# Optimization experiments

Hardware: AMD Instinct MI355X
Metric: run time of the kernel (lower is better)

## Reference

```python
import jax, jax.numpy as jnp
import numpy as np

B, N, C = 2, 2048, 1024
H = 16
D = C // H  # head_dim = 64

def setup_inputs() -> dict:
    key = jax.random.key(0)
    ks = jax.random.split(key, 5)
    scale = 1.0 / np.sqrt(C)
    return {
        "x": jax.random.normal(ks[0], (B, N, C), dtype=jnp.float32),
        "w_qkv": jax.random.normal(ks[1], (C, 3 * C), dtype=jnp.float32) * scale,
        "b_qkv": jnp.zeros((3 * C,), dtype=jnp.float32),
        "w_out": jax.random.normal(ks[2], (C, C), dtype=jnp.float32) * scale,
        "b_out": jnp.zeros((C,), dtype=jnp.float32),
    }

def reference(x, w_qkv, b_qkv, w_out, b_out):
    b, n, c = x.shape
    # fused QKV projection: [B,N,3C] -> [3,B,H,N,D]
    qkv = (x @ w_qkv + b_qkv).reshape(b, n, 3, H, D).transpose(2, 0, 3, 1, 4)
    q, k, v = qkv[0], qkv[1], qkv[2]
    # scaled dot-product attention (dropout is identity in eval / p=0)
    attn = jnp.einsum('bhqd,bhkd->bhqk', q, k) * (D ** -0.5)
    attn = jax.nn.softmax(attn, axis=-1)
    out = jnp.einsum('bhqk,bhkd->bhqd', attn, v)
    out = out.transpose(0, 2, 1, 3).reshape(b, n, c)
    return out @ w_out + b_out
```

## Files before the change

kernel.cpp:

```cpp
#include <hip/hip_runtime.h>

typedef unsigned short u16;
typedef __bf16 bf16x8 __attribute__((ext_vector_type(8)));
typedef __bf16 bf16x4 __attribute__((ext_vector_type(4)));
typedef float f32x4 __attribute__((ext_vector_type(4)));

#define LOG2E 1.44269504088896340736f

constexpr int Bc = 2, Nc = 2048, Cch = 1024, Hh = 16, Dd = 64;
constexpr int Mrows = Bc * Nc;
constexpr int N_QKV = 3 * Cch;

__device__ __forceinline__ u16 f2bf(float f) {
  unsigned int u = __float_as_uint(f);
  u += 0x7fffu + ((u >> 16) & 1u);
  return (u16)(u >> 16);
}

__device__ __forceinline__ void gload16(const void* g, void* l) {
  __builtin_amdgcn_global_load_lds((const __attribute__((address_space(1))) void*)g,
                                   (__attribute__((address_space(3))) void*)l, 16, 0, 0);
}

#define MFMA(a, b, c) __builtin_amdgcn_mfma_f32_16x16x32_bf16(a, b, c, 0, 0, 0)

__global__ __launch_bounds__(256) void cast_x_kernel(const float* __restrict__ in,
                                                     u16* __restrict__ out, int n4) {
  int i = blockIdx.x * 256 + threadIdx.x;
  if (i >= n4) return;
  float4 v = *(const float4*)&in[i * 4];
  union { u16 h[4]; short4 s; } u;
  u.h[0] = f2bf(v.x); u.h[1] = f2bf(v.y); u.h[2] = f2bf(v.z); u.h[3] = f2bf(v.w);
  *(short4*)&out[i * 4] = u.s;
}

__global__ __launch_bounds__(256) void transpose_cast_kernel(const float* __restrict__ in,
                                                             u16* __restrict__ out,
                                                             int R, int Cq) {
  __shared__ float tile[32][33];
  int bx = blockIdx.x * 32;
  int by = blockIdx.y * 32;
  int tx = threadIdx.x & 31, ty = threadIdx.x >> 5;
#pragma unroll
  for (int i = 0; i < 32; i += 8)
    tile[ty + i][tx] = in[(size_t)(by + ty + i) * Cq + bx + tx];
  __syncthreads();
#pragma unroll
  for (int i = 0; i < 32; i += 8)
    out[(size_t)(bx + ty + i) * R + by + tx] = f2bf(tile[tx][ty + i]);
}

__global__ __launch_bounds__(256) void transpose_v_kernel(const u16* __restrict__ in,
                                                          u16* __restrict__ out) {
  __shared__ u16 tile[32][33];
  int n0 = blockIdx.x * 32, d0 = blockIdx.y * 32;
  size_t base = (size_t)blockIdx.z * 2048 * 64;
  int tx = threadIdx.x & 31, ty = threadIdx.x >> 5;
#pragma unroll
  for (int i = 0; i < 32; i += 8)
    tile[ty + i][tx] = in[base + (size_t)(n0 + ty + i) * 64 + d0 + tx];
  __syncthreads();
#pragma unroll
  for (int i = 0; i < 32; i += 8)
    out[base + (size_t)(d0 + ty + i) * 2048 + n0 + tx] = tile[tx][ty + i];
}

template <int NWG, int NY>
__global__ __launch_bounds__(256) void gemm_qkv_kernel(const u16* __restrict__ A,
                                                       const u16* __restrict__ Bt,
                                                       const float* __restrict__ bias,
                                                       u16* __restrict__ Qo,
                                                       u16* __restrict__ Ko,
                                                       u16* __restrict__ Vo) {
  __shared__ u16 As[128 * 32];
  __shared__ u16 Bs[128 * 32];
  f32x4 acc[4][4] = {};
  int tid = threadIdx.x, lane = tid & 63, wid = tid >> 6;
  int wr = wid >> 1, wc = wid & 1;
  int l15 = lane & 15, g = lane >> 4;
  int wgid = (blockIdx.x & 7) * (NWG >> 3) + (blockIdx.x >> 3);
  int rowBase = (wgid / NY) * 128, colBase = (wgid % NY) * 128;
  int rowS = tid >> 2, c8 = (tid & 3) << 3;

  for (int k0 = 0; k0 < 1024; k0 += 32) {
    __syncthreads();
    gload16(&A[(size_t)(rowBase + rowS) * 1024 + k0 + c8],        (char*)As + wid * 1024);
    gload16(&A[(size_t)(rowBase + 64 + rowS) * 1024 + k0 + c8],   (char*)As + 4096 + wid * 1024);
    gload16(&Bt[(size_t)(colBase + rowS) * 1024 + k0 + c8],       (char*)Bs + wid * 1024);
    gload16(&Bt[(size_t)(colBase + 64 + rowS) * 1024 + k0 + c8],  (char*)Bs + 4096 + wid * 1024);
    __syncthreads();
    bf16x8 af[4], bfv[4];
#pragma unroll
    for (int m = 0; m < 4; ++m)
      af[m] = *(const bf16x8*)&As[(wr * 64 + m * 16 + l15) * 32 + g * 8];
#pragma unroll
    for (int n = 0; n < 4; ++n)
      bfv[n] = *(const bf16x8*)&Bs[(wc * 64 + n * 16 + l15) * 32 + g * 8];
#pragma unroll
    for (int m = 0; m < 4; ++m)
#pragma unroll
      for (int n = 0; n < 4; ++n)
        acc[m][n] = MFMA(af[m], bfv[n], acc[m][n]);
  }

#pragma unroll
  for (int m = 0; m < 4; ++m)
#pragma unroll
    for (int n = 0; n < 4; ++n) {
      int colc = colBase + wc * 64 + n * 16 + l15;
      float bv = bias[colc];
      int s = colc >> 10, hd = colc & 1023;
      int h = hd >> 6, d = hd & 63;
      float scale = (s == 0) ? (0.125f * LOG2E) : 1.0f;
#pragma unroll
      for (int j = 0; j < 4; ++j) {
        int r = rowBase + wr * 64 + m * 16 + g * 4 + j;
        int b = r >> 11, nn = r & 2047;
        u16 v = f2bf((acc[m][n][j] + bv) * scale);
        size_t idx = (((size_t)(b * 16 + h)) * 2048 + nn) * 64 + d;
        if (s == 0)      Qo[idx] = v;
        else if (s == 1) Ko[idx] = v;
        else             Vo[idx] = v;
      }
    }
}

__global__ __launch_bounds__(256) void attn_kernel(const u16* __restrict__ Q,
                                                   const u16* __restrict__ Km,
                                                   const u16* __restrict__ Vt,
                                                   u16* __restrict__ AO) {
  __shared__ u16 KV[16384];
  __shared__ u16 Ps[128 * 72];
  int tid = threadIdx.x, lane = tid & 63, w = tid >> 6;
  int l15 = lane & 15, g = lane >> 4;
  int r8 = lane >> 3;
  int src_col = (((lane & 7) ^ (r8 & 7)) << 4);
  int r7q = l15 & 7;
  int bidw = ((blockIdx.x & 7) << 6) + (blockIdx.x >> 3);
  int bh = bidw >> 4, qt = bidw & 15;
  int b = bh >> 4, h = bh & 15;
  const size_t base = (size_t)bh * 2048 * 64;
  const char* Kg = (const char*)(Km + base);
  const char* Vg = (const char*)(Vt + base);
  int qrow0 = qt * 128 + w * 32;

  bf16x8 qf[2][2];
#pragma unroll
  for (int mm = 0; mm < 2; ++mm)
#pragma unroll
    for (int ks = 0; ks < 2; ++ks)
      qf[mm][ks] = *(const bf16x8*)&Q[base + (size_t)(qrow0 + mm * 16 + l15) * 64 + ks * 32 + g * 8];

#define STAGE(cb, nk)                                                          \
  do {                                                                         \
    int kr = (nk) + w * 8 + r8;                                                \
    gload16(Kg + (size_t)kr * 128 + src_col,                                   \
            (char*)KV + (cb) * 8192 + w * 1024);                               \
    gload16(Kg + (size_t)(kr + 32) * 128 + src_col,                            \
            (char*)KV + (cb) * 8192 + 4096 + w * 1024);                        \
    int vr = w * 8 + r8;                                                       \
    gload16(Vg + (size_t)vr * 4096 + (nk) * 2 + src_col,                       \
            (char*)KV + 16384 + (cb) * 8192 + w * 1024);                       \
    gload16(Vg + (size_t)(vr + 32) * 4096 + (nk) * 2 + src_col,                \
            (char*)KV + 16384 + (cb) * 8192 + 4096 + w * 1024);                \
  } while (0)

  f32x4 o[2][4] = {};
  float lacc[2] = {0.f, 0.f};
  int xk[2] = {((0 + g) ^ r7q) << 4, ((4 + g) ^ r7q) << 4};

  STAGE(0, 0);

  for (int t = 0; t < 32; ++t) {
    int cur = t & 1;
    int nk_next = ((t + 1) & 31) * 64;
    STAGE(cur ^ 1, nk_next);
    asm volatile("s_waitcnt vmcnt(4)" ::: "memory");
    __builtin_amdgcn_s_barrier();
    asm volatile("" ::: "memory");

    const char* bK = (const char*)KV + cur * 8192;
    const char* bV = (const char*)KV + 16384 + cur * 8192;

    f32x4 st[2][4] = {};
#pragma unroll
    for (int ks = 0; ks < 2; ++ks) {
      bf16x8 kf[4];
#pragma unroll
      for (int n = 0; n < 4; ++n)
        kf[n] = *(const bf16x8*)(bK + (n * 16 + l15) * 128 + xk[ks]);
#pragma unroll
      for (int mm = 0; mm < 2; ++mm)
#pragma unroll
        for (int n = 0; n < 4; ++n)
          st[mm][n] = MFMA(kf[n], qf[mm][ks], st[mm][n]);
    }

#pragma unroll
    for (int mm = 0; mm < 2; ++mm) {
      f32x4 sum4 = {0.f, 0.f, 0.f, 0.f};
#pragma unroll
      for (int n = 0; n < 4; ++n) {
#pragma unroll
        for (int j = 0; j < 4; ++j) {
          float p;
          asm("v_exp_f32 %0, %1" : "=v"(p) : "v"(st[mm][n][j]));
          st[mm][n][j] = p;
        }
        sum4 += st[mm][n];
      }
      lacc[mm] += (sum4[0] + sum4[1]) + (sum4[2] + sum4[3]);
#pragma unroll
      for (int n = 0; n < 4; ++n) {
        bf16x4 pv;
#pragma unroll
        for (int j = 0; j < 4; ++j) pv[j] = (__bf16)st[mm][n][j];
        *(bf16x4*)&Ps[(w * 32 + mm * 16 + l15) * 72 + n * 16 + g * 4] = pv;
      }
    }

#pragma unroll
    for (int ks = 0; ks < 2; ++ks) {
      bf16x8 pf[2];
#pragma unroll
      for (int mm = 0; mm < 2; ++mm)
        pf[mm] = *(const bf16x8*)&Ps[(w * 32 + mm * 16 + l15) * 72 + ks * 32 + g * 8];
#pragma unroll
      for (int dn = 0; dn < 4; ++dn) {
        bf16x8 vf = *(const bf16x8*)(bV + (dn * 16 + l15) * 128 + xk[ks]);
#pragma unroll
        for (int mm = 0; mm < 2; ++mm)
          o[mm][dn] = MFMA(vf, pf[mm], o[mm][dn]);
      }
    }
    asm volatile("" ::: "memory");
    __builtin_amdgcn_s_barrier();
  }
#undef STAGE

#pragma unroll
  for (int mm = 0; mm < 2; ++mm) {
    float l0 = lacc[mm];
    l0 += __shfl_xor(l0, 16);
    l0 += __shfl_xor(l0, 32);
    float inv = 1.0f / l0;
    int nq = qrow0 + mm * 16 + l15;
    size_t rowb = ((size_t)b * 2048 + nq) * 1024 + h * 64;
#pragma unroll
    for (int dn = 0; dn < 4; ++dn) {
      bf16x4 ov;
#pragma unroll
      for (int j = 0; j < 4; ++j) ov[j] = (__bf16)(o[mm][dn][j] * inv);
      *(bf16x4*)&AO[rowb + dn * 16 + g * 4] = ov;
    }
  }
}

template <int NWG, int NY>
__global__ __launch_bounds__(256) void gemm_proj_kernel(const u16* __restrict__ A,
                                                        const u16* __restrict__ Bt,
                                                        const float* __restrict__ bias,
                                                        float* __restrict__ out) {
  __shared__ u16 As[128 * 32];
  __shared__ u16 Bs[128 * 32];
  f32x4 acc[4][4] = {};
  int tid = threadIdx.x, lane = tid & 63, wid = tid >> 6;
  int wr = wid >> 1, wc = wid & 1;
  int l15 = lane & 15, g = lane >> 4;
  int wgid = (blockIdx.x & 7) * (NWG >> 3) + (blockIdx.x >> 3);
  int rowBase = (wgid / NY) * 128, colBase = (wgid % NY) * 128;
  int rowS = tid >> 2, c8 = (tid & 3) << 3;

  for (int k0 = 0; k0 < 1024; k0 += 32) {
    __syncthreads();
    gload16(&A[(size_t)(rowBase + rowS) * 1024 + k0 + c8],        (char*)As + wid * 1024);
    gload16(&A[(size_t)(rowBase + 64 + rowS) * 1024 + k0 + c8],   (char*)As + 4096 + wid * 1024);
    gload16(&Bt[(size_t)(colBase + rowS) * 1024 + k0 + c8],       (char*)Bs + wid * 1024);
    gload16(&Bt[(size_t)(colBase + 64 + rowS) * 1024 + k0 + c8],  (char*)Bs + 4096 + wid * 1024);
    __syncthreads();
    bf16x8 af[4], bfv[4];
#pragma unroll
    for (int m = 0; m < 4; ++m)
      af[m] = *(const bf16x8*)&As[(wr * 64 + m * 16 + l15) * 32 + g * 8];
#pragma unroll
    for (int n = 0; n < 4; ++n)
      bfv[n] = *(const bf16x8*)&Bs[(wc * 64 + n * 16 + l15) * 32 + g * 8];
#pragma unroll
    for (int m = 0; m < 4; ++m)
#pragma unroll
      for (int n = 0; n < 4; ++n)
        acc[m][n] = MFMA(af[m], bfv[n], acc[m][n]);
  }

#pragma unroll
  for (int m = 0; m < 4; ++m)
#pragma unroll
    for (int n = 0; n < 4; ++n) {
      int colc = colBase + wc * 64 + n * 16 + l15;
      float bv = bias[colc];
#pragma unroll
      for (int j = 0; j < 4; ++j) {
        int r = rowBase + wr * 64 + m * 16 + g * 4 + j;
        out[(size_t)r * 1024 + colc] = acc[m][n][j] + bv;
      }
    }
}

extern "C" void kernel_launch(void* const* d_in, const int* in_sizes, int n_in,
                              void* d_out, int out_size, void* d_ws, size_t ws_size,
                              hipStream_t stream) {
  const float* x     = (const float*)d_in[0];
  const float* w_qkv = (const float*)d_in[1];
  const float* b_qkv = (const float*)d_in[2];
  const float* w_out = (const float*)d_in[3];
  const float* b_out = (const float*)d_in[4];
  float* out = (float*)d_out;

  char* w = (char*)d_ws;
  u16* Xb  = (u16*)(w);
  u16* W1T = (u16*)(w + (8u << 20));
  u16* W2T = (u16*)(w + (14u << 20));
  u16* Qb  = (u16*)(w + (16u << 20));
  u16* Kb  = (u16*)(w + (24u << 20));
  u16* Vtb = (u16*)(w + (32u << 20));
  u16* AO  = (u16*)(w + (40u << 20));
  u16* Vb  = (u16*)(w + (48u << 20));

  cast_x_kernel<<<4096, 256, 0, stream>>>(x, Xb, Mrows * Cch / 4);
  transpose_cast_kernel<<<dim3(N_QKV / 32, Cch / 32), 256, 0, stream>>>(w_qkv, W1T, Cch, N_QKV);
  transpose_cast_kernel<<<dim3(Cch / 32, Cch / 32), 256, 0, stream>>>(w_out, W2T, Cch, Cch);
  gemm_qkv_kernel<768, 24><<<768, 256, 0, stream>>>(Xb, W1T, b_qkv, Qb, Kb, Vb);
  transpose_v_kernel<<<dim3(64, 2, 32), 256, 0, stream>>>(Vb, Vtb);
  attn_kernel<<<512, 256, 0, stream>>>(Qb, Kb, Vtb, AO);
  gemm_proj_kernel<256, 8><<<256, 256, 0, stream>>>(AO, W2T, b_out, out);

  (void)in_sizes; (void)n_in; (void)out_size; (void)ws_size;
}
```

Baseline: 204.6 us.

## Double GEMM K-tile to 64 with XOR-swizzled LDS and finer projection tiles

Both GEMMs now stage 64-wide K slices per barrier pair instead of 32, halving the number of synchronizations and global-to-LDS rounds. The LDS layout is XOR-swizzled in 16-byte chunks to avoid bank conflicts on the fragment reads. The output projection switches to 128x64 tiles with 512 workgroups, so its grid covers more of the CUs, at the cost of reloading A more often. LDS usage per block doubles.

```diff
diff --git a/kernel.cpp b/kernel.cpp
--- a/kernel.cpp
+++ b/kernel.cpp
@@ -72,35 +72,44 @@
                                                        u16* __restrict__ Qo,
                                                        u16* __restrict__ Ko,
                                                        u16* __restrict__ Vo) {
-  __shared__ u16 As[128 * 32];
-  __shared__ u16 Bs[128 * 32];
+  __shared__ u16 As[128 * 64];
+  __shared__ u16 Bs[128 * 64];
   f32x4 acc[4][4] = {};
   int tid = threadIdx.x, lane = tid & 63, wid = tid >> 6;
   int wr = wid >> 1, wc = wid & 1;
   int l15 = lane & 15, g = lane >> 4;
+  int r8 = lane >> 3;
+  int src_col = ((lane & 7) ^ r8) << 4;
   int wgid = (blockIdx.x & 7) * (NWG >> 3) + (blockIdx.x >> 3);
   int rowBase = (wgid / NY) * 128, colBase = (wgid % NY) * 128;
-  int rowS = tid >> 2, c8 = (tid & 3) << 3;
-
-  for (int k0 = 0; k0 < 1024; k0 += 32) {
+  int xa[2] = {((0 + g) ^ (l15 & 7)) << 4, ((4 + g) ^ (l15 & 7)) << 4};
+
+  for (int k0 = 0; k0 < 1024; k0 += 64) {
     __syncthreads();
-    gload16(&A[(size_t)(rowBase + rowS) * 1024 + k0 + c8],        (char*)As + wid * 1024);
-    gload16(&A[(size_t)(rowBase + 64 + rowS) * 1024 + k0 + c8],   (char*)As + 4096 + wid * 1024);
-    gload16(&Bt[(size_t)(colBase + rowS) * 1024 + k0 + c8],       (char*)Bs + wid * 1024);
-    gload16(&Bt[(size_t)(colBase + 64 + rowS) * 1024 + k0 + c8],  (char*)Bs + 4096 + wid * 1024);
+#pragma unroll
+    for (int r = 0; r < 4; ++r) {
+      int row = wid * 8 + r8 + 32 * r;
+      gload16((const char*)&A[(size_t)(rowBase + row) * 1024 + k0] + src_col,
+              (char*)As + r * 4096 + wid * 1024);
+      gload16((const char*)&Bt[(size_t)(colBase + row) * 1024 + k0] + src_col,
+              (char*)Bs + r * 4096 + wid * 1024);
+    }
     __syncthreads();
-    bf16x8 af[4], bfv[4];
-#pragma unroll
-    for (int m = 0; m < 4; ++m)
-      af[m] = *(const bf16x8*)&As[(wr * 64 + m * 16 + l15) * 32 + g * 8];
-#pragma unroll
-    for (int n = 0; n < 4; ++n)
-      bfv[n] = *(const bf16x8*)&Bs[(wc * 64 + n * 16 + l15) * 32 + g * 8];
-#pragma unroll
-    for (int m = 0; m < 4; ++m)
+#pragma unroll
+    for (int kk = 0; kk < 2; ++kk) {
+      bf16x8 af[4], bfv[4];
+#pragma unroll
+      for (int m = 0; m < 4; ++m)
+        af[m] = *(const bf16x8*)((const char*)As + (wr * 64 + m * 16 + l15) * 128 + xa[kk]);
 #pragma unroll
       for (int n = 0; n < 4; ++n)
-        acc[m][n] = MFMA(af[m], bfv[n], acc[m][n]);
+        bfv[n] = *(const bf16x8*)((const char*)Bs + (wc * 64 + n * 16 + l15) * 128 + xa[kk]);
+#pragma unroll
+      for (int m = 0; m < 4; ++m)
+#pragma unroll
+        for (int n = 0; n < 4; ++n)
+          acc[m][n] = MFMA(af[m], bfv[n], acc[m][n]);
+    }
   }
 
 #pragma unroll
@@ -261,46 +270,55 @@
                                                         const u16* __restrict__ Bt,
                                                         const float* __restrict__ bias,
                                                         float* __restrict__ out) {
-  __shared__ u16 As[128 * 32];
-  __shared__ u16 Bs[128 * 32];
-  f32x4 acc[4][4] = {};
+  __shared__ u16 As[128 * 64];
+  __shared__ u16 Bs[64 * 64];
+  f32x4 acc[2][4] = {};
   int tid = threadIdx.x, lane = tid & 63, wid = tid >> 6;
-  int wr = wid >> 1, wc = wid & 1;
   int l15 = lane & 15, g = lane >> 4;
+  int r8 = lane >> 3;
+  int src_col = ((lane & 7) ^ r8) << 4;
   int wgid = (blockIdx.x & 7) * (NWG >> 3) + (blockIdx.x >> 3);
-  int rowBase = (wgid / NY) * 128, colBase = (wgid % NY) * 128;
-  int rowS = tid >> 2, c8 = (tid & 3) << 3;
-
-  for (int k0 = 0; k0 < 1024; k0 += 32) {
+  int rowBase = (wgid / NY) * 128, colBase = (wgid % NY) * 64;
+  int xa[2] = {((0 + g) ^ (l15 & 7)) << 4, ((4 + g) ^ (l15 & 7)) << 4};
+
+  for (int k0 = 0; k0 < 1024; k0 += 64) {
     __syncthreads();
-    gload16(&A[(size_t)(rowBase + rowS) * 1024 + k0 + c8],        (char*)As + wid * 1024);
-    gload16(&A[(size_t)(rowBase + 64 + rowS) * 1024 + k0 + c8],   (char*)As + 4096 + wid * 1024);
-    gload16(&Bt[(size_t)(colBase + rowS) * 1024 + k0 + c8],       (char*)Bs + wid * 1024);
-    gload16(&Bt[(size_t)(colBase + 64 + rowS) * 1024 + k0 + c8],  (char*)Bs + 4096 + wid * 1024);
+#pragma unroll
+    for (int r = 0; r < 4; ++r) {
+      int row = wid * 8 + r8 + 32 * r;
+      gload16((const char*)&A[(size_t)(rowBase + row) * 1024 + k0] + src_col,
+              (char*)As + r * 4096 + wid * 1024);
+      if (r < 2)
+        gload16((const char*)&Bt[(size_t)(colBase + row) * 1024 + k0] + src_col,
+                (char*)Bs + r * 4096 + wid * 1024);
+    }
     __syncthreads();
-    bf16x8 af[4], bfv[4];
-#pragma unroll
-    for (int m = 0; m < 4; ++m)
-      af[m] = *(const bf16x8*)&As[(wr * 64 + m * 16 + l15) * 32 + g * 8];
-#pragma unroll
-    for (int n = 0; n < 4; ++n)
-      bfv[n] = *(const bf16x8*)&Bs[(wc * 64 + n * 16 + l15) * 32 + g * 8];
-#pragma unroll
-    for (int m = 0; m < 4; ++m)
+#pragma unroll
+    for (int kk = 0; kk < 2; ++kk) {
+      bf16x8 af[2], bfv[4];
+#pragma unroll
+      for (int m = 0; m < 2; ++m)
+        af[m] = *(const bf16x8*)((const char*)As + (wid * 32 + m * 16 + l15) * 128 + xa[kk]);
 #pragma unroll
       for (int n = 0; n < 4; ++n)
-        acc[m][n] = MFMA(af[m], bfv[n], acc[m][n]);
+        bfv[n] = *(const bf16x8*)((const char*)Bs + (n * 16 + l15) * 128 + xa[kk]);
+#pragma unroll
+      for (int m = 0; m < 2; ++m)
+#pragma unroll
+        for (int n = 0; n < 4; ++n)
+          acc[m][n] = MFMA(af[m], bfv[n], acc[m][n]);
+    }
   }
 
 #pragma unroll
-  for (int m = 0; m < 4; ++m)
+  for (int m = 0; m < 2; ++m)
 #pragma unroll
     for (int n = 0; n < 4; ++n) {
-      int colc = colBase + wc * 64 + n * 16 + l15;
+      int colc = colBase + n * 16 + l15;
       float bv = bias[colc];
 #pragma unroll
       for (int j = 0; j < 4; ++j) {
-        int r = rowBase + wr * 64 + m * 16 + g * 4 + j;
+        int r = rowBase + wid * 32 + m * 16 + g * 4 + j;
         out[(size_t)r * 1024 + colc] = acc[m][n][j] + bv;
       }
     }
@@ -332,7 +350,7 @@
   gemm_qkv_kernel<768, 24><<<768, 256, 0, stream>>>(Xb, W1T, b_qkv, Qb, Kb, Vb);
   transpose_v_kernel<<<dim3(64, 2, 32), 256, 0, stream>>>(Vb, Vtb);
   attn_kernel<<<512, 256, 0, stream>>>(Qb, Kb, Vtb, AO);
-  gemm_proj_kernel<256, 8><<<256, 256, 0, stream>>>(AO, W2T, b_out, out);
+  gemm_proj_kernel<512, 16><<<512, 256, 0, stream>>>(AO, W2T, b_out, out);
 
   (void)in_sizes; (void)n_in; (void)out_size; (void)ws_size;
 }
```

New measurement: 207.0 us. No clear change (+1.2%).
